# Optimization experiments

Hardware: AMD Instinct MI355X
Metric: run time of the kernel (lower is better)

Reference implementation:

```python
import jax, jax.numpy as jnp
import numpy as np


def setup_inputs() -> dict:
    key = jax.random.key(0)
    kq, kk, kv = jax.random.split(key, 3)
    B, H, S, D = 2, 16, 2048, 64
    Q = jax.random.normal(kq, (B, H, S, D), dtype=jnp.float32)
    K = jax.random.normal(kk, (B, H, S, D), dtype=jnp.float32)
    V = jax.random.normal(kv, (B, H, S, D), dtype=jnp.float32)
    return {"Q": Q, "K": K, "V": V}


def reference(Q, K, V):
    # Faithful to the torch module: NO 1/sqrt(d_k) scaling (d_k is computed
    # but never used in the original forward).
    scores = jnp.einsum('bhqd,bhkd->bhqk', Q, K)      # [B,H,S,S]
    attn = jax.nn.softmax(scores, axis=-1)
    out = jnp.einsum('bhqk,bhkd->bhqd', attn, V)      # [B,H,S,D]
    return out
```

## Files before the change

kernel.cpp:

```cpp
#include <hip/hip_runtime.h>


typedef __bf16    bf16_t;
typedef _Float16  f16_t;
typedef __bf16    bf16x8 __attribute__((ext_vector_type(8)));
typedef _Float16  f16x8  __attribute__((ext_vector_type(8)));
typedef float     f32x4  __attribute__((ext_vector_type(4)));

constexpr int S  = 2048;
constexpr int Dh = 64;
constexpr int KT = 64;
constexpr int QT = 128;
constexpr float LOG2E = 1.44269504088896340736f;

__device__ __forceinline__ int sw(int row, int col) {
    return row * 64 + ((((col >> 3) ^ (row & 7)) << 3) | (col & 7));
}

__device__ __forceinline__ int swp(int row, int k) {
    return sw(row >> 1, (row & 1) * 32 + k);
}

template<int SN>
__global__ __launch_bounds__(256, 4)
void attn_kernel(const float* __restrict__ Qg,
                 const float* __restrict__ Kg,
                 const float* __restrict__ Vg,
                 float* __restrict__ Og,
                 float* __restrict__ Opart,
                 float* __restrict__ lpart)
{
    __shared__ alignas(16) f16_t  Khs[KT * Dh];
    __shared__ alignas(16) bf16_t Vts[Dh * KT];
    __shared__ alignas(16) bf16_t Pbs[64 * 64];

    const int tid  = threadIdx.x;
    const int lane = tid & 63;
    const int wv   = tid >> 6;
    const int l15  = lane & 15;
    const int qd   = lane >> 4;
    const int wb   = wv * 32;

    const int bx   = blockIdx.x;
    const int head = bx & 31;
    const int r5   = bx >> 5;
    const int qt   = r5 / SN;
    const int half = r5 % SN;
    const int tile = head * 16 + qt;
    const int ch0  = (SN == 3) ? half * 11 : half * 16;
    const int nch  = (SN == 3) ? (half == 2 ? 10 : 11) : (SN == 2 ? 16 : 32);

    const float* Qp = Qg + (size_t)tile * QT * Dh;
    const float* Kp = Kg + (size_t)head * S * Dh;
    const float* Vp = Vg + (size_t)head * S * Dh;

    const int skey = tid >> 4;
    const int sc4  = (tid & 15) * 4;
    const int vkb  = (tid >> 4) * 4;
    const int vc4  = (tid & 15) * 4;

    f16x8 qf[2][2];
    #pragma unroll
    for (int sub = 0; sub < 2; ++sub) {
        const float* qrow = Qp + (size_t)(wb + sub * 16 + l15) * Dh;
        #pragma unroll
        for (int ks = 0; ks < 2; ++ks) {
            const float* p = qrow + ks * 32 + qd * 8;
            const float4 a = *(const float4*)(p);
            const float4 b = *(const float4*)(p + 4);
            const float xs[8] = {a.x, a.y, a.z, a.w, b.x, b.y, b.z, b.w};
            #pragma unroll
            for (int j = 0; j < 8; ++j) qf[sub][ks][j] = (f16_t)(xs[j] * LOG2E);
        }
    }

    f32x4 oa[2][4];
    float lp[2];
    #pragma unroll
    for (int s2 = 0; s2 < 2; ++s2) {
        lp[s2] = 0.f;
        #pragma unroll
        for (int t = 0; t < 4; ++t) oa[s2][t] = (f32x4){0.f, 0.f, 0.f, 0.f};
    }

    float4 kbuf[4], vbuf[4];
    {
        const float* Kc = Kp + (size_t)ch0 * KT * Dh;
        const float* Vc = Vp + (size_t)ch0 * KT * Dh;
        #pragma unroll
        for (int it = 0; it < 4; ++it)
            kbuf[it] = *(const float4*)(Kc + (size_t)(it * 16 + skey) * Dh + sc4);
        #pragma unroll
        for (int i = 0; i < 4; ++i)
            vbuf[i] = *(const float4*)(Vc + (size_t)(vkb + i) * Dh + vc4);
    }

    #pragma unroll 1
    for (int ci = 0; ci < nch; ++ci) {
        __syncthreads();

        #pragma unroll
        for (int it = 0; it < 4; ++it) {
            const float xs[4] = {kbuf[it].x, kbuf[it].y, kbuf[it].z, kbuf[it].w};
            union { f16_t h[4]; uint2 u; } ph;
            #pragma unroll
            for (int j = 0; j < 4; ++j) ph.h[j] = (f16_t)xs[j];
            *(uint2*)&Khs[sw(it * 16 + skey, sc4)] = ph.u;
        }
        {
            const float rs[4][4] = {{vbuf[0].x, vbuf[1].x, vbuf[2].x, vbuf[3].x},
                                    {vbuf[0].y, vbuf[1].y, vbuf[2].y, vbuf[3].y},
                                    {vbuf[0].z, vbuf[1].z, vbuf[2].z, vbuf[3].z},
                                    {vbuf[0].w, vbuf[1].w, vbuf[2].w, vbuf[3].w}};
            #pragma unroll
            for (int i = 0; i < 4; ++i) {
                union { bf16_t h[4]; uint2 u; } pv;
                #pragma unroll
                for (int j = 0; j < 4; ++j) pv.h[j] = (bf16_t)rs[i][j];
                *(uint2*)&Vts[sw(vc4 + i, vkb)] = pv.u;
            }
        }
        __syncthreads();

        if (ci + 1 < nch) {
            const float* Kc = Kp + (size_t)(ch0 + ci + 1) * KT * Dh;
            const float* Vc = Vp + (size_t)(ch0 + ci + 1) * KT * Dh;
            #pragma unroll
            for (int it = 0; it < 4; ++it)
                kbuf[it] = *(const float4*)(Kc + (size_t)(it * 16 + skey) * Dh + sc4);
            #pragma unroll
            for (int i = 0; i < 4; ++i)
                vbuf[i] = *(const float4*)(Vc + (size_t)(vkb + i) * Dh + vc4);
        }

        #pragma unroll
        for (int np = 0; np < 2; ++np) {
            f32x4 st[2][2];
            #pragma unroll
            for (int s2 = 0; s2 < 2; ++s2)
                #pragma unroll
                for (int t = 0; t < 2; ++t) st[s2][t] = (f32x4){0.f, 0.f, 0.f, 0.f};
            __builtin_amdgcn_s_setprio(1);
            #pragma unroll
            for (int ks = 0; ks < 2; ++ks) {
                const int co = ks * 32 + qd * 8;
                const f16x8 ak0 = *(const f16x8*)&Khs[sw((np * 2 + 0) * 16 + l15, co)];
                const f16x8 ak1 = *(const f16x8*)&Khs[sw((np * 2 + 1) * 16 + l15, co)];
                #pragma unroll
                for (int s2 = 0; s2 < 2; ++s2) {
                    st[s2][0] = __builtin_amdgcn_mfma_f32_16x16x32_f16(ak0, qf[s2][ks], st[s2][0], 0, 0, 0);
                    st[s2][1] = __builtin_amdgcn_mfma_f32_16x16x32_f16(ak1, qf[s2][ks], st[s2][1], 0, 0, 0);
                }
            }
            __builtin_amdgcn_s_setprio(0);
            #pragma unroll
            for (int s2 = 0; s2 < 2; ++s2) {
                #pragma unroll
                for (int t = 0; t < 2; ++t) {
                    union { bf16_t h[4]; uint2 u; } pb;
                    #pragma unroll
                    for (int r = 0; r < 4; ++r) {
                        const float e = __builtin_amdgcn_exp2f(st[s2][t][r]);
                        lp[s2] += e;
                        pb.h[r] = (bf16_t)e;
                    }
                    *(uint2*)&Pbs[swp(wb + s2 * 16 + l15, t * 16 + qd * 4)] = pb.u;
                }
            }
            const int co = np * 32 + qd * 8;
            const bf16x8 pa0 = *(const bf16x8*)&Pbs[swp(wb + l15,      qd * 8)];
            const bf16x8 pa1 = *(const bf16x8*)&Pbs[swp(wb + 16 + l15, qd * 8)];
            __builtin_amdgcn_s_setprio(1);
            #pragma unroll
            for (int dt = 0; dt < 4; ++dt) {
                const bf16x8 vb = *(const bf16x8*)&Vts[sw(dt * 16 + l15, co)];
                oa[0][dt] = __builtin_amdgcn_mfma_f32_16x16x32_bf16(pa0, vb, oa[0][dt], 0, 0, 0);
                oa[1][dt] = __builtin_amdgcn_mfma_f32_16x16x32_bf16(pa1, vb, oa[1][dt], 0, 0, 0);
            }
            __builtin_amdgcn_s_setprio(0);
        }
    }

    #pragma unroll
    for (int s2 = 0; s2 < 2; ++s2) {
        lp[s2] += __shfl_xor(lp[s2], 16, 64);
        lp[s2] += __shfl_xor(lp[s2], 32, 64);
    }

    if (SN > 1) {
        float* Po = Opart + (size_t)(tile * SN + half) * (QT * Dh);
        float* lq = lpart + (size_t)(tile * SN + half) * QT;
        #pragma unroll
        for (int s2 = 0; s2 < 2; ++s2) {
            if (qd == 0) lq[wb + s2 * 16 + l15] = lp[s2];
            #pragma unroll
            for (int r = 0; r < 4; ++r) {
                const int row = wb + s2 * 16 + qd * 4 + r;
                #pragma unroll
                for (int dt = 0; dt < 4; ++dt)
                    Po[(size_t)row * Dh + dt * 16 + l15] = oa[s2][dt][r];
            }
        }
    } else {
        float* Op = Og + (size_t)tile * QT * Dh;
        #pragma unroll
        for (int s2 = 0; s2 < 2; ++s2) {
            #pragma unroll
            for (int r = 0; r < 4; ++r) {
                const float inv = 1.0f / __shfl(lp[s2], qd * 4 + r, 64);
                const int row = wb + s2 * 16 + qd * 4 + r;
                #pragma unroll
                for (int dt = 0; dt < 4; ++dt)
                    Op[(size_t)row * Dh + dt * 16 + l15] = oa[s2][dt][r] * inv;
            }
        }
    }
}

template<int SN>
__global__ __launch_bounds__(256)
void combine_kernel(const float* __restrict__ Opart,
                    const float* __restrict__ lpart,
                    float* __restrict__ Og)
{
    const int i  = blockIdx.x * 256 + threadIdx.x;
    const int q  = i >> 11;
    const int rw = (i >> 4) & 127;
    const size_t e = (size_t)(i & 2047) * 4;
    float4 acc = {0.f, 0.f, 0.f, 0.f};
    float  l   = 0.f;
    #pragma unroll
    for (int h = 0; h < SN; ++h) {
        const float4 a = *(const float4*)(Opart + (size_t)(q * SN + h) * (QT * Dh) + e);
        l += lpart[(size_t)(q * SN + h) * QT + rw];
        acc.x += a.x; acc.y += a.y; acc.z += a.z; acc.w += a.w;
    }
    const float inv = 1.0f / l;
    float4 o;
    o.x = acc.x * inv; o.y = acc.y * inv; o.z = acc.z * inv; o.w = acc.w * inv;
    *(float4*)(Og + (size_t)i * 4) = o;
}

extern "C" void kernel_launch(void* const* d_in, const int* in_sizes, int n_in,
                              void* d_out, int out_size, void* d_ws, size_t ws_size,
                              hipStream_t stream)
{
    const float* Q = (const float*)d_in[0];
    const float* K = (const float*)d_in[1];
    const float* V = (const float*)d_in[2];
    float*       O = (float*)d_out;

    constexpr size_t TILE_O = (size_t)QT * Dh;
    constexpr size_t NEED3  = (512ull * 3 * (TILE_O + QT)) * sizeof(float);
    constexpr size_t NEED2  = (512ull * 2 * (TILE_O + QT)) * sizeof(float);
    const int n4 = (int)(512 * TILE_O / 4);

    if (ws_size >= NEED3) {
        float* Opart = (float*)d_ws;
        float* lpart = Opart + 512ull * 3 * TILE_O;
        attn_kernel<3><<<dim3(1536), dim3(256), 0, stream>>>(
            Q, K, V, nullptr, Opart, lpart);
        combine_kernel<3><<<dim3(n4 / 256), dim3(256), 0, stream>>>(Opart, lpart, O);
    } else if (ws_size >= NEED2) {
        float* Opart = (float*)d_ws;
        float* lpart = Opart + 512ull * 2 * TILE_O;
        attn_kernel<2><<<dim3(1024), dim3(256), 0, stream>>>(
            Q, K, V, nullptr, Opart, lpart);
        combine_kernel<2><<<dim3(n4 / 256), dim3(256), 0, stream>>>(Opart, lpart, O);
    } else {
        attn_kernel<1><<<dim3(512), dim3(256), 0, stream>>>(
            Q, K, V, O, nullptr, nullptr);
    }
}
```

Measured before the change: 143.4 us.

## Switch to 32x32x16 MFMA and pass P through registers via permlane32_swap

Replaces the 16x16x32 MFMA tiling with 32x32x16 MFMAs for both QK^T and PV. The exponentiated probabilities are now rearranged into the PV operand layout in registers using permlane32_swap, so the Pbs shared-memory staging buffer and its store/load round trip are gone. This cuts LDS traffic and shared memory per block, and the row-sum reduction needs fewer shuffles. In exchange the larger accumulator tiles change register usage and the output store pattern.

```diff
diff --git a/kernel.cpp b/kernel.cpp
--- a/kernel.cpp
+++ b/kernel.cpp
@@ -5,7 +5,8 @@
 typedef _Float16  f16_t;
 typedef __bf16    bf16x8 __attribute__((ext_vector_type(8)));
 typedef _Float16  f16x8  __attribute__((ext_vector_type(8)));
-typedef float     f32x4  __attribute__((ext_vector_type(4)));
+typedef float     f32x16 __attribute__((ext_vector_type(16)));
+typedef int       int2v  __attribute__((ext_vector_type(2)));
 
 constexpr int S  = 2048;
 constexpr int Dh = 64;
@@ -17,8 +18,10 @@
     return row * 64 + ((((col >> 3) ^ (row & 7)) << 3) | (col & 7));
 }
 
-__device__ __forceinline__ int swp(int row, int k) {
-    return sw(row >> 1, (row & 1) * 32 + k);
+__device__ __forceinline__ unsigned pkbf(float a, float b) {
+    union { bf16_t h[2]; unsigned u; } t;
+    t.h[0] = (bf16_t)a; t.h[1] = (bf16_t)b;
+    return t.u;
 }
 
 template<int SN>
@@ -32,13 +35,12 @@
 {
     __shared__ alignas(16) f16_t  Khs[KT * Dh];
     __shared__ alignas(16) bf16_t Vts[Dh * KT];
-    __shared__ alignas(16) bf16_t Pbs[64 * 64];
 
     const int tid  = threadIdx.x;
     const int lane = tid & 63;
     const int wv   = tid >> 6;
-    const int l15  = lane & 15;
-    const int qd   = lane >> 4;
+    const int l31  = lane & 31;
+    const int h    = lane >> 5;
     const int wb   = wv * 32;
 
     const int bx   = blockIdx.x;
@@ -59,29 +61,26 @@
     const int vkb  = (tid >> 4) * 4;
     const int vc4  = (tid & 15) * 4;
 
-    f16x8 qf[2][2];
-    #pragma unroll
-    for (int sub = 0; sub < 2; ++sub) {
-        const float* qrow = Qp + (size_t)(wb + sub * 16 + l15) * Dh;
-        #pragma unroll
-        for (int ks = 0; ks < 2; ++ks) {
-            const float* p = qrow + ks * 32 + qd * 8;
+    f16x8 qf[4];
+    {
+        const float* qrow = Qp + (size_t)(wb + l31) * Dh;
+        #pragma unroll
+        for (int ds = 0; ds < 4; ++ds) {
+            const float* p = qrow + ds * 16 + h * 8;
             const float4 a = *(const float4*)(p);
             const float4 b = *(const float4*)(p + 4);
             const float xs[8] = {a.x, a.y, a.z, a.w, b.x, b.y, b.z, b.w};
             #pragma unroll
-            for (int j = 0; j < 8; ++j) qf[sub][ks][j] = (f16_t)(xs[j] * LOG2E);
-        }
-    }
-
-    f32x4 oa[2][4];
-    float lp[2];
+            for (int j = 0; j < 8; ++j) qf[ds][j] = (f16_t)(xs[j] * LOG2E);
+        }
+    }
+
+    f32x16 oa[2];
     #pragma unroll
-    for (int s2 = 0; s2 < 2; ++s2) {
-        lp[s2] = 0.f;
-        #pragma unroll
-        for (int t = 0; t < 4; ++t) oa[s2][t] = (f32x4){0.f, 0.f, 0.f, 0.f};
-    }
+    for (int db = 0; db < 2; ++db)
+        #pragma unroll
+        for (int r = 0; r < 16; ++r) oa[db][r] = 0.f;
+    float lp = 0.f;
 
     float4 kbuf[4], vbuf[4];
     {
@@ -102,9 +101,9 @@
         #pragma unroll
         for (int it = 0; it < 4; ++it) {
             const float xs[4] = {kbuf[it].x, kbuf[it].y, kbuf[it].z, kbuf[it].w};
-            union { f16_t h[4]; uint2 u; } ph;
-            #pragma unroll
-            for (int j = 0; j < 4; ++j) ph.h[j] = (f16_t)xs[j];
+            union { f16_t h4[4]; uint2 u; } ph;
+            #pragma unroll
+            for (int j = 0; j < 4; ++j) ph.h4[j] = (f16_t)xs[j];
             *(uint2*)&Khs[sw(it * 16 + skey, sc4)] = ph.u;
         }
         {
@@ -114,9 +113,9 @@
                                     {vbuf[0].w, vbuf[1].w, vbuf[2].w, vbuf[3].w}};
             #pragma unroll
             for (int i = 0; i < 4; ++i) {
-                union { bf16_t h[4]; uint2 u; } pv;
+                union { bf16_t h4[4]; uint2 u; } pv;
                 #pragma unroll
-                for (int j = 0; j < 4; ++j) pv.h[j] = (bf16_t)rs[i][j];
+                for (int j = 0; j < 4; ++j) pv.h4[j] = (bf16_t)rs[i][j];
                 *(uint2*)&Vts[sw(vc4 + i, vkb)] = pv.u;
             }
         }
@@ -134,85 +133,69 @@
         }
 
         #pragma unroll
-        for (int np = 0; np < 2; ++np) {
-            f32x4 st[2][2];
-            #pragma unroll
-            for (int s2 = 0; s2 < 2; ++s2)
+        for (int kb = 0; kb < 2; ++kb) {
+            f32x16 st;
+            #pragma unroll
+            for (int r = 0; r < 16; ++r) st[r] = 0.f;
+            __builtin_amdgcn_s_setprio(1);
+            #pragma unroll
+            for (int ds = 0; ds < 4; ++ds) {
+                const f16x8 ak = *(const f16x8*)&Khs[sw(kb * 32 + l31, ds * 16 + h * 8)];
+                st = __builtin_amdgcn_mfma_f32_32x32x16_f16(ak, qf[ds], st, 0, 0, 0);
+            }
+            __builtin_amdgcn_s_setprio(0);
+            float e[16];
+            #pragma unroll
+            for (int r = 0; r < 16; ++r) {
+                e[r] = __builtin_amdgcn_exp2f(st[r]);
+                lp += e[r];
+            }
+            #pragma unroll
+            for (int ksl = 0; ksl < 2; ++ksl) {
+                const int b = ksl * 8;
+                const unsigned c0 = pkbf(e[b + 0], e[b + 1]);
+                const unsigned c1 = pkbf(e[b + 2], e[b + 3]);
+                const unsigned c2 = pkbf(e[b + 4], e[b + 5]);
+                const unsigned c3 = pkbf(e[b + 6], e[b + 7]);
+                const int2v s02 = __builtin_amdgcn_permlane32_swap((int)c0, (int)c2, false, false);
+                const int2v s13 = __builtin_amdgcn_permlane32_swap((int)c1, (int)c3, false, false);
+                union { unsigned u[4]; bf16x8 v; } pa;
+                pa.u[0] = (unsigned)s02.x;
+                pa.u[1] = (unsigned)s13.x;
+                pa.u[2] = (unsigned)s02.y;
+                pa.u[3] = (unsigned)s13.y;
+                __builtin_amdgcn_s_setprio(1);
                 #pragma unroll
-                for (int t = 0; t < 2; ++t) st[s2][t] = (f32x4){0.f, 0.f, 0.f, 0.f};
-            __builtin_amdgcn_s_setprio(1);
-            #pragma unroll
-            for (int ks = 0; ks < 2; ++ks) {
-                const int co = ks * 32 + qd * 8;
-                const f16x8 ak0 = *(const f16x8*)&Khs[sw((np * 2 + 0) * 16 + l15, co)];
-                const f16x8 ak1 = *(const f16x8*)&Khs[sw((np * 2 + 1) * 16 + l15, co)];
-                #pragma unroll
-                for (int s2 = 0; s2 < 2; ++s2) {
-                    st[s2][0] = __builtin_amdgcn_mfma_f32_16x16x32_f16(ak0, qf[s2][ks], st[s2][0], 0, 0, 0);
-                    st[s2][1] = __builtin_amdgcn_mfma_f32_16x16x32_f16(ak1, qf[s2][ks], st[s2][1], 0, 0, 0);
+                for (int db = 0; db < 2; ++db) {
+                    const bf16x8 vb = *(const bf16x8*)&Vts[sw(db * 32 + l31, kb * 32 + ksl * 16 + h * 8)];
+                    oa[db] = __builtin_amdgcn_mfma_f32_32x32x16_bf16(pa.v, vb, oa[db], 0, 0, 0);
                 }
-            }
-            __builtin_amdgcn_s_setprio(0);
-            #pragma unroll
-            for (int s2 = 0; s2 < 2; ++s2) {
-                #pragma unroll
-                for (int t = 0; t < 2; ++t) {
-                    union { bf16_t h[4]; uint2 u; } pb;
-                    #pragma unroll
-                    for (int r = 0; r < 4; ++r) {
-                        const float e = __builtin_amdgcn_exp2f(st[s2][t][r]);
-                        lp[s2] += e;
-                        pb.h[r] = (bf16_t)e;
-                    }
-                    *(uint2*)&Pbs[swp(wb + s2 * 16 + l15, t * 16 + qd * 4)] = pb.u;
-                }
-            }
-            const int co = np * 32 + qd * 8;
-            const bf16x8 pa0 = *(const bf16x8*)&Pbs[swp(wb + l15,      qd * 8)];
-            const bf16x8 pa1 = *(const bf16x8*)&Pbs[swp(wb + 16 + l15, qd * 8)];
-            __builtin_amdgcn_s_setprio(1);
-            #pragma unroll
-            for (int dt = 0; dt < 4; ++dt) {
-                const bf16x8 vb = *(const bf16x8*)&Vts[sw(dt * 16 + l15, co)];
-                oa[0][dt] = __builtin_amdgcn_mfma_f32_16x16x32_bf16(pa0, vb, oa[0][dt], 0, 0, 0);
-                oa[1][dt] = __builtin_amdgcn_mfma_f32_16x16x32_bf16(pa1, vb, oa[1][dt], 0, 0, 0);
-            }
-            __builtin_amdgcn_s_setprio(0);
-        }
-    }
-
-    #pragma unroll
-    for (int s2 = 0; s2 < 2; ++s2) {
-        lp[s2] += __shfl_xor(lp[s2], 16, 64);
-        lp[s2] += __shfl_xor(lp[s2], 32, 64);
-    }
+                __builtin_amdgcn_s_setprio(0);
+            }
+        }
+    }
+
+    lp += __shfl_xor(lp, 32, 64);
 
     if (SN > 1) {
         float* Po = Opart + (size_t)(tile * SN + half) * (QT * Dh);
         float* lq = lpart + (size_t)(tile * SN + half) * QT;
-        #pragma unroll
-        for (int s2 = 0; s2 < 2; ++s2) {
-            if (qd == 0) lq[wb + s2 * 16 + l15] = lp[s2];
-            #pragma unroll
-            for (int r = 0; r < 4; ++r) {
-                const int row = wb + s2 * 16 + qd * 4 + r;
-                #pragma unroll
-                for (int dt = 0; dt < 4; ++dt)
-                    Po[(size_t)row * Dh + dt * 16 + l15] = oa[s2][dt][r];
-            }
+        if (lane < 32) lq[wb + lane] = lp;
+        #pragma unroll
+        for (int r = 0; r < 16; ++r) {
+            const int row = wb + (r & 3) + 8 * (r >> 2) + 4 * h;
+            Po[(size_t)row * Dh +      l31] = oa[0][r];
+            Po[(size_t)row * Dh + 32 + l31] = oa[1][r];
         }
     } else {
         float* Op = Og + (size_t)tile * QT * Dh;
         #pragma unroll
-        for (int s2 = 0; s2 < 2; ++s2) {
-            #pragma unroll
-            for (int r = 0; r < 4; ++r) {
-                const float inv = 1.0f / __shfl(lp[s2], qd * 4 + r, 64);
-                const int row = wb + s2 * 16 + qd * 4 + r;
-                #pragma unroll
-                for (int dt = 0; dt < 4; ++dt)
-                    Op[(size_t)row * Dh + dt * 16 + l15] = oa[s2][dt][r] * inv;
-            }
+        for (int r = 0; r < 16; ++r) {
+            const int rowq = (r & 3) + 8 * (r >> 2) + 4 * h;
+            const float inv = 1.0f / __shfl(lp, rowq, 64);
+            const int row = wb + rowq;
+            Op[(size_t)row * Dh +      l31] = oa[0][r] * inv;
+            Op[(size_t)row * Dh + 32 + l31] = oa[1][r] * inv;
         }
     }
 }
@@ -230,9 +213,9 @@
     float4 acc = {0.f, 0.f, 0.f, 0.f};
     float  l   = 0.f;
     #pragma unroll
-    for (int h = 0; h < SN; ++h) {
-        const float4 a = *(const float4*)(Opart + (size_t)(q * SN + h) * (QT * Dh) + e);
-        l += lpart[(size_t)(q * SN + h) * QT + rw];
+    for (int hh = 0; hh < SN; ++hh) {
+        const float4 a = *(const float4*)(Opart + (size_t)(q * SN + hh) * (QT * Dh) + e);
+        l += lpart[(size_t)(q * SN + hh) * QT + rw];
         acc.x += a.x; acc.y += a.y; acc.z += a.z; acc.w += a.w;
     }
     const float inv = 1.0f / l;
```

New measurement: 146.3 us. Within noise of the previous version (+2.0%).

## Precompute swizzled fp16/bf16 K and V in a prep kernel

Applied to the files above, without the earlier changes.

Adds a prep kernel that converts K to fp16 and V to transposed bf16 in the swizzled LDS layout once per head, and stores them in the workspace. The attention kernel then loads these 16-bit tiles with plain 128-bit copies into shared memory. This halves K/V load bytes and removes the repeated conversion and transpose done by each of the many query-tile blocks. The cost is an extra launch and pass over K/V, plus a larger workspace requirement; the old path remains as a fallback.

```diff
diff --git a/kernel.cpp b/kernel.cpp
--- a/kernel.cpp
+++ b/kernel.cpp
@@ -21,11 +21,55 @@
     return sw(row >> 1, (row & 1) * 32 + k);
 }
 
-template<int SN>
+__global__ __launch_bounds__(256)
+void prep_kernel(const float* __restrict__ Kg, const float* __restrict__ Vg,
+                 f16_t* __restrict__ Kpre, bf16_t* __restrict__ Vpre)
+{
+    const int tid  = threadIdx.x;
+    const int bx   = blockIdx.x;
+    const int head = bx & 31;
+    const int ch   = bx >> 5;
+    const size_t off = (size_t)(head * 32 + ch) * (KT * Dh);
+    const float* Kc = Kg + off;
+    const float* Vc = Vg + off;
+    f16_t*  Ko = Kpre + off;
+    bf16_t* Vo = Vpre + off;
+
+    const int skey = tid >> 4;
+    const int sc4  = (tid & 15) * 4;
+    #pragma unroll
+    for (int it = 0; it < 4; ++it) {
+        const float4 k4 = *(const float4*)(Kc + (size_t)(it * 16 + skey) * Dh + sc4);
+        const float xs[4] = {k4.x, k4.y, k4.z, k4.w};
+        union { f16_t h[4]; uint2 u; } ph;
+        #pragma unroll
+        for (int j = 0; j < 4; ++j) ph.h[j] = (f16_t)xs[j];
+        *(uint2*)&Ko[sw(it * 16 + skey, sc4)] = ph.u;
+    }
+    const int vkb = (tid >> 4) * 4;
+    const int vc4 = (tid & 15) * 4;
+    float4 vb4[4];
+    #pragma unroll
+    for (int i = 0; i < 4; ++i)
+        vb4[i] = *(const float4*)(Vc + (size_t)(vkb + i) * Dh + vc4);
+    const float rs[4][4] = {{vb4[0].x, vb4[1].x, vb4[2].x, vb4[3].x},
+                            {vb4[0].y, vb4[1].y, vb4[2].y, vb4[3].y},
+                            {vb4[0].z, vb4[1].z, vb4[2].z, vb4[3].z},
+                            {vb4[0].w, vb4[1].w, vb4[2].w, vb4[3].w}};
+    #pragma unroll
+    for (int i = 0; i < 4; ++i) {
+        union { bf16_t h[4]; uint2 u; } pv;
+        #pragma unroll
+        for (int j = 0; j < 4; ++j) pv.h[j] = (bf16_t)rs[i][j];
+        *(uint2*)&Vo[sw(vc4 + i, vkb)] = pv.u;
+    }
+}
+
+template<int SN, bool PRE>
 __global__ __launch_bounds__(256, 4)
 void attn_kernel(const float* __restrict__ Qg,
-                 const float* __restrict__ Kg,
-                 const float* __restrict__ Vg,
+                 const void* __restrict__ Kin,
+                 const void* __restrict__ Vin,
                  float* __restrict__ Og,
                  float* __restrict__ Opart,
                  float* __restrict__ lpart)
@@ -51,8 +95,6 @@
     const int nch  = (SN == 3) ? (half == 2 ? 10 : 11) : (SN == 2 ? 16 : 32);
 
     const float* Qp = Qg + (size_t)tile * QT * Dh;
-    const float* Kp = Kg + (size_t)head * S * Dh;
-    const float* Vp = Vg + (size_t)head * S * Dh;
 
     const int skey = tid >> 4;
     const int sc4  = (tid & 15) * 4;
@@ -83,10 +125,16 @@
         for (int t = 0; t < 4; ++t) oa[s2][t] = (f32x4){0.f, 0.f, 0.f, 0.f};
     }
 
+    uint4  pk[2], pv4[2];
     float4 kbuf[4], vbuf[4];
-    {
-        const float* Kc = Kp + (size_t)ch0 * KT * Dh;
-        const float* Vc = Vp + (size_t)ch0 * KT * Dh;
+    if constexpr (PRE) {
+        const uint4* Kc = (const uint4*)Kin + (size_t)(head * 32 + ch0) * 512;
+        const uint4* Vc = (const uint4*)Vin + (size_t)(head * 32 + ch0) * 512;
+        pk[0]  = Kc[tid]; pk[1]  = Kc[tid + 256];
+        pv4[0] = Vc[tid]; pv4[1] = Vc[tid + 256];
+    } else {
+        const float* Kc = (const float*)Kin + (size_t)(head * 32 + ch0) * (KT * Dh);
+        const float* Vc = (const float*)Vin + (size_t)(head * 32 + ch0) * (KT * Dh);
         #pragma unroll
         for (int it = 0; it < 4; ++it)
             kbuf[it] = *(const float4*)(Kc + (size_t)(it * 16 + skey) * Dh + sc4);
@@ -99,38 +147,48 @@
     for (int ci = 0; ci < nch; ++ci) {
         __syncthreads();
 
-        #pragma unroll
-        for (int it = 0; it < 4; ++it) {
-            const float xs[4] = {kbuf[it].x, kbuf[it].y, kbuf[it].z, kbuf[it].w};
-            union { f16_t h[4]; uint2 u; } ph;
-            #pragma unroll
-            for (int j = 0; j < 4; ++j) ph.h[j] = (f16_t)xs[j];
-            *(uint2*)&Khs[sw(it * 16 + skey, sc4)] = ph.u;
-        }
-        {
+        if constexpr (PRE) {
+            ((uint4*)Khs)[tid] = pk[0];  ((uint4*)Khs)[tid + 256] = pk[1];
+            ((uint4*)Vts)[tid] = pv4[0]; ((uint4*)Vts)[tid + 256] = pv4[1];
+        } else {
+            #pragma unroll
+            for (int it = 0; it < 4; ++it) {
+                const float xs[4] = {kbuf[it].x, kbuf[it].y, kbuf[it].z, kbuf[it].w};
+                union { f16_t h[4]; uint2 u; } ph;
+                #pragma unroll
+                for (int j = 0; j < 4; ++j) ph.h[j] = (f16_t)xs[j];
+                *(uint2*)&Khs[sw(it * 16 + skey, sc4)] = ph.u;
+            }
             const float rs[4][4] = {{vbuf[0].x, vbuf[1].x, vbuf[2].x, vbuf[3].x},
                                     {vbuf[0].y, vbuf[1].y, vbuf[2].y, vbuf[3].y},
                                     {vbuf[0].z, vbuf[1].z, vbuf[2].z, vbuf[3].z},
                                     {vbuf[0].w, vbuf[1].w, vbuf[2].w, vbuf[3].w}};
             #pragma unroll
             for (int i = 0; i < 4; ++i) {
-                union { bf16_t h[4]; uint2 u; } pv;
-                #pragma unroll
-                for (int j = 0; j < 4; ++j) pv.h[j] = (bf16_t)rs[i][j];
-                *(uint2*)&Vts[sw(vc4 + i, vkb)] = pv.u;
+                union { bf16_t h[4]; uint2 u; } pvv;
+                #pragma unroll
+                for (int j = 0; j < 4; ++j) pvv.h[j] = (bf16_t)rs[i][j];
+                *(uint2*)&Vts[sw(vc4 + i, vkb)] = pvv.u;
             }
         }
         __syncthreads();
 
         if (ci + 1 < nch) {
-            const float* Kc = Kp + (size_t)(ch0 + ci + 1) * KT * Dh;
-            const float* Vc = Vp + (size_t)(ch0 + ci + 1) * KT * Dh;
-            #pragma unroll
-            for (int it = 0; it < 4; ++it)
-                kbuf[it] = *(const float4*)(Kc + (size_t)(it * 16 + skey) * Dh + sc4);
-            #pragma unroll
-            for (int i = 0; i < 4; ++i)
-                vbuf[i] = *(const float4*)(Vc + (size_t)(vkb + i) * Dh + vc4);
+            if constexpr (PRE) {
+                const uint4* Kc = (const uint4*)Kin + (size_t)(head * 32 + ch0 + ci + 1) * 512;
+                const uint4* Vc = (const uint4*)Vin + (size_t)(head * 32 + ch0 + ci + 1) * 512;
+                pk[0]  = Kc[tid]; pk[1]  = Kc[tid + 256];
+                pv4[0] = Vc[tid]; pv4[1] = Vc[tid + 256];
+            } else {
+                const float* Kc = (const float*)Kin + (size_t)(head * 32 + ch0 + ci + 1) * (KT * Dh);
+                const float* Vc = (const float*)Vin + (size_t)(head * 32 + ch0 + ci + 1) * (KT * Dh);
+                #pragma unroll
+                for (int it = 0; it < 4; ++it)
+                    kbuf[it] = *(const float4*)(Kc + (size_t)(it * 16 + skey) * Dh + sc4);
+                #pragma unroll
+                for (int i = 0; i < 4; ++i)
+                    vbuf[i] = *(const float4*)(Vc + (size_t)(vkb + i) * Dh + vc4);
+            }
         }
 
         #pragma unroll
@@ -251,24 +309,37 @@
     float*       O = (float*)d_out;
 
     constexpr size_t TILE_O = (size_t)QT * Dh;
-    constexpr size_t NEED3  = (512ull * 3 * (TILE_O + QT)) * sizeof(float);
+    constexpr size_t OP3    = 512ull * 3 * TILE_O;
+    constexpr size_t LP3    = 512ull * 3 * QT;
+    constexpr size_t NEED3  = (OP3 + LP3) * sizeof(float);
     constexpr size_t NEED2  = (512ull * 2 * (TILE_O + QT)) * sizeof(float);
+    constexpr size_t KVPRE_ELEMS = 32ull * S * Dh;
+    constexpr size_t KV_BYTES    = 2 * KVPRE_ELEMS * 2;
     const int n4 = (int)(512 * TILE_O / 4);
 
-    if (ws_size >= NEED3) {
+    if (ws_size >= NEED3 + KV_BYTES) {
+        float*  Opart = (float*)d_ws;
+        float*  lpart = Opart + OP3;
+        f16_t*  Kpre  = (f16_t*)(lpart + LP3);
+        bf16_t* Vpre  = (bf16_t*)(Kpre + KVPRE_ELEMS);
+        prep_kernel<<<dim3(1024), dim3(256), 0, stream>>>(K, V, Kpre, Vpre);
+        attn_kernel<3, true><<<dim3(1536), dim3(256), 0, stream>>>(
+            Q, Kpre, Vpre, nullptr, Opart, lpart);
+        combine_kernel<3><<<dim3(n4 / 256), dim3(256), 0, stream>>>(Opart, lpart, O);
+    } else if (ws_size >= NEED3) {
         float* Opart = (float*)d_ws;
-        float* lpart = Opart + 512ull * 3 * TILE_O;
-        attn_kernel<3><<<dim3(1536), dim3(256), 0, stream>>>(
+        float* lpart = Opart + OP3;
+        attn_kernel<3, false><<<dim3(1536), dim3(256), 0, stream>>>(
             Q, K, V, nullptr, Opart, lpart);
         combine_kernel<3><<<dim3(n4 / 256), dim3(256), 0, stream>>>(Opart, lpart, O);
     } else if (ws_size >= NEED2) {
         float* Opart = (float*)d_ws;
         float* lpart = Opart + 512ull * 2 * TILE_O;
-        attn_kernel<2><<<dim3(1024), dim3(256), 0, stream>>>(
+        attn_kernel<2, false><<<dim3(1024), dim3(256), 0, stream>>>(
             Q, K, V, nullptr, Opart, lpart);
         combine_kernel<2><<<dim3(n4 / 256), dim3(256), 0, stream>>>(Opart, lpart, O);
     } else {
-        attn_kernel<1><<<dim3(512), dim3(256), 0, stream>>>(
+        attn_kernel<1, false><<<dim3(512), dim3(256), 0, stream>>>(
             Q, K, V, O, nullptr, nullptr);
     }
 }
```

Result: slower. 191.0 us (+33.2%).

## Fuse split-KV combine into attention kernel via last-arriving-block counter

Applied to the files above, without the earlier changes.

Each split block publishes its partial output and row sums, then atomically increments a per-tile counter. The last block to arrive for a tile sums all partials, normalizes them and writes the final output, so the separate combine kernel launch is no longer needed. The cost is a memset on the counters, thread fences, and a serialized tail of work in whichever block arrives last.

```diff
diff --git a/kernel.cpp b/kernel.cpp
--- a/kernel.cpp
+++ b/kernel.cpp
@@ -21,14 +21,15 @@
     return sw(row >> 1, (row & 1) * 32 + k);
 }
 
-template<int SN>
+template<int SN, bool FUSE>
 __global__ __launch_bounds__(256, 4)
 void attn_kernel(const float* __restrict__ Qg,
                  const float* __restrict__ Kg,
                  const float* __restrict__ Vg,
                  float* __restrict__ Og,
                  float* __restrict__ Opart,
-                 float* __restrict__ lpart)
+                 float* __restrict__ lpart,
+                 int*   __restrict__ cnt)
 {
     __shared__ alignas(16) f16_t  Khs[KT * Dh];
     __shared__ alignas(16) bf16_t Vts[Dh * KT];
@@ -199,6 +200,39 @@
                 #pragma unroll
                 for (int dt = 0; dt < 4; ++dt)
                     Po[(size_t)row * Dh + dt * 16 + l15] = oa[s2][dt][r];
+            }
+        }
+        if constexpr (FUSE) {
+            __threadfence();
+            __shared__ int lastarrive;
+            if (tid == 0) lastarrive = atomicAdd(&cnt[tile], 1);
+            __syncthreads();
+            if (lastarrive == SN - 1) {
+                __threadfence();
+                __shared__ float linv[QT];
+                if (tid < QT) {
+                    float l = 0.f;
+                    #pragma unroll
+                    for (int h2 = 0; h2 < SN; ++h2)
+                        l += lpart[(size_t)(tile * SN + h2) * QT + tid];
+                    linv[tid] = 1.0f / l;
+                }
+                __syncthreads();
+                float4* Ot = (float4*)(Og + (size_t)tile * (QT * Dh));
+                #pragma unroll
+                for (int k2 = 0; k2 < (QT * Dh / 4) / 256; ++k2) {
+                    const int i = tid + k2 * 256;
+                    float4 acc = {0.f, 0.f, 0.f, 0.f};
+                    #pragma unroll
+                    for (int h2 = 0; h2 < SN; ++h2) {
+                        const float4 a = *((const float4*)(Opart
+                            + (size_t)(tile * SN + h2) * (QT * Dh)) + i);
+                        acc.x += a.x; acc.y += a.y; acc.z += a.z; acc.w += a.w;
+                    }
+                    const float iv = linv[i >> 4];
+                    acc.x *= iv; acc.y *= iv; acc.z *= iv; acc.w *= iv;
+                    Ot[i] = acc;
+                }
             }
         }
     } else {
@@ -251,24 +285,43 @@
     float*       O = (float*)d_out;
 
     constexpr size_t TILE_O = (size_t)QT * Dh;
-    constexpr size_t NEED3  = (512ull * 3 * (TILE_O + QT)) * sizeof(float);
-    constexpr size_t NEED2  = (512ull * 2 * (TILE_O + QT)) * sizeof(float);
+    constexpr size_t OP3 = 512ull * 3 * TILE_O;
+    constexpr size_t LP3 = 512ull * 3 * QT;
+    constexpr size_t OP2 = 512ull * 2 * TILE_O;
+    constexpr size_t LP2 = 512ull * 2 * QT;
+    constexpr size_t CNT_BYTES = 512 * sizeof(int);
+    constexpr size_t NEED3 = (OP3 + LP3) * sizeof(float);
+    constexpr size_t NEED2 = (OP2 + LP2) * sizeof(float);
     const int n4 = (int)(512 * TILE_O / 4);
 
-    if (ws_size >= NEED3) {
+    if (ws_size >= NEED3 + CNT_BYTES) {
         float* Opart = (float*)d_ws;
-        float* lpart = Opart + 512ull * 3 * TILE_O;
-        attn_kernel<3><<<dim3(1536), dim3(256), 0, stream>>>(
-            Q, K, V, nullptr, Opart, lpart);
+        float* lpart = Opart + OP3;
+        int*   cnt   = (int*)(lpart + LP3);
+        hipMemsetAsync(cnt, 0, CNT_BYTES, stream);
+        attn_kernel<3, true><<<dim3(1536), dim3(256), 0, stream>>>(
+            Q, K, V, O, Opart, lpart, cnt);
+    } else if (ws_size >= NEED3) {
+        float* Opart = (float*)d_ws;
+        float* lpart = Opart + OP3;
+        attn_kernel<3, false><<<dim3(1536), dim3(256), 0, stream>>>(
+            Q, K, V, nullptr, Opart, lpart, nullptr);
         combine_kernel<3><<<dim3(n4 / 256), dim3(256), 0, stream>>>(Opart, lpart, O);
+    } else if (ws_size >= NEED2 + CNT_BYTES) {
+        float* Opart = (float*)d_ws;
+        float* lpart = Opart + OP2;
+        int*   cnt   = (int*)(lpart + LP2);
+        hipMemsetAsync(cnt, 0, CNT_BYTES, stream);
+        attn_kernel<2, true><<<dim3(1024), dim3(256), 0, stream>>>(
+            Q, K, V, O, Opart, lpart, cnt);
     } else if (ws_size >= NEED2) {
         float* Opart = (float*)d_ws;
-        float* lpart = Opart + 512ull * 2 * TILE_O;
-        attn_kernel<2><<<dim3(1024), dim3(256), 0, stream>>>(
-            Q, K, V, nullptr, Opart, lpart);
+        float* lpart = Opart + OP2;
+        attn_kernel<2, false><<<dim3(1024), dim3(256), 0, stream>>>(
+            Q, K, V, nullptr, Opart, lpart, nullptr);
         combine_kernel<2><<<dim3(n4 / 256), dim3(256), 0, stream>>>(Opart, lpart, O);
     } else {
-        attn_kernel<1><<<dim3(512), dim3(256), 0, stream>>>(
-            Q, K, V, O, nullptr, nullptr);
-    }
-}
+        attn_kernel<1, false><<<dim3(512), dim3(256), 0, stream>>>(
+            Q, K, V, O, nullptr, nullptr, nullptr);
+    }
+}
```

Result: slower. 422.2 us (+194.4%).
